# Optimization experiments

Hardware: AMD Instinct MI355X
Metric: run time of the kernel (lower is better)

The kernel has to match this reference:

```python
import jax, jax.numpy as jnp
import numpy as np

VOCAB = 50257
D = 256
N_UTT = 64
L = 512


def gru_scan(x, W_ih, W_hh, b_ih, b_hh):
    # torch nn.GRU (single layer, batch_first) semantics.
    # x: [B, T, d] -> outputs [B, T, d]
    B, T, d = x.shape
    gx = jnp.einsum('btd,gd->btg', x, W_ih) + b_ih  # [B, T, 3d] input gates precomputed
    gx = jnp.transpose(gx, (1, 0, 2))               # [T, B, 3d] for scan over time

    def step(h, gxt):
        gh = h @ W_hh.T + b_hh                      # [B, 3d]
        xr, xz, xn = jnp.split(gxt, 3, axis=-1)
        hr, hz, hn = jnp.split(gh, 3, axis=-1)
        r = jax.nn.sigmoid(xr + hr)
        z = jax.nn.sigmoid(xz + hz)
        n = jnp.tanh(xn + r * hn)
        h_new = (1.0 - z) * n + z * h
        return h_new, h_new

    h0 = jnp.zeros((B, d), x.dtype)
    _, hs = jax.lax.scan(step, h0, gx)              # hs: [T, B, d]
    return jnp.transpose(hs, (1, 0, 2))


def attn_pool(out, w, b):
    # out: [B, T, d]; Linear(d,1) -> softmax over T -> weighted sum
    logits = out @ w + b                            # [B, T]
    weights = jax.nn.softmax(logits, axis=-1)
    return jnp.einsum('bt,btd->bd', weights, out)   # [B, d]


def setup_inputs() -> dict:
    key = jax.random.key(0)
    ks = jax.random.split(key, 16)
    s = 1.0 / np.sqrt(D)
    u = lambda k, shape: jax.random.uniform(k, shape, jnp.float32, -s, s)
    return {
        'tokens': jax.random.randint(ks[0], (N_UTT, L), 0, VOCAB, dtype=jnp.int32),
        'embed': jax.random.normal(ks[1], (VOCAB, D), jnp.float32),
        'wg_Wih': u(ks[2], (3 * D, D)),
        'wg_Whh': u(ks[3], (3 * D, D)),
        'wg_bih': u(ks[4], (3 * D,)),
        'wg_bhh': u(ks[5], (3 * D,)),
        'ua_w': u(ks[6], (D,)),
        'ua_b': u(ks[7], ()),
        'sg_Wih': u(ks[8], (3 * D, D)),
        'sg_Whh': u(ks[9], (3 * D, D)),
        'sg_bih': u(ks[10], (3 * D,)),
        'sg_bhh': u(ks[11], (3 * D,)),
        'da_w': u(ks[12], (D,)),
        'da_b': u(ks[13], ()),
    }


def reference(tokens, embed, wg_Wih, wg_Whh, wg_bih, wg_bhh, ua_w, ua_b,
              sg_Wih, sg_Whh, sg_bih, sg_bhh, da_w, da_b):
    # Word level: embed each utterance, GRU, attention pooling (batched over utterances)
    emb = embed[tokens]                                   # [N, L, d]
    word_out = gru_scan(emb, wg_Wih, wg_Whh, wg_bih, wg_bhh)
    utt_vecs = attn_pool(word_out, ua_w, ua_b)            # [N, d]
    # Sentence level: pad_sequence of [1,d] vectors -> [N, 1, d] (batch=N, seq=1)
    sent_in = utt_vecs[:, None, :]                        # [N, 1, d]
    sent_out = gru_scan(sent_in, sg_Wih, sg_Whh, sg_bih, sg_bhh)
    dialog_vec = attn_pool(sent_out, da_w, da_b)          # [N, d] (softmax over seq len 1)
    return dialog_vec
```

## Files before the change

kernel.cpp:

```cpp
#include <hip/hip_runtime.h>

typedef _Float16 f16x8 __attribute__((ext_vector_type(8)));
typedef float f32x4 __attribute__((ext_vector_type(4)));

constexpr int D = 256;
constexpr int NUTT = 64;
constexpr int L = 512;
constexpr int G = 768;
constexpr int CHUNK = 128;
constexpr int NCH = L / CHUNK;
constexpr int NBLK = 6;
constexpr int NGEMM = NCH * NUTT * NBLK;

__device__ __forceinline__ void lds_barrier() {
  asm volatile("s_waitcnt lgkmcnt(0)\n\ts_barrier" ::: "memory");
}

__device__ __forceinline__ float fast_rcp(float x) {
  return __builtin_amdgcn_rcpf(x);
}
__device__ __forceinline__ float sigm(float x) {
  return fast_rcp(1.0f + __expf(-x));
}
__device__ __forceinline__ float tanh_f(float x) {
  float ax = fabsf(x);
  float e = __expf(-2.0f * ax);
  float r = (1.0f - e) * fast_rcp(1.0f + e);
  return copysignf(r, x);
}

__global__ __launch_bounds__(256) void pack_wih(
    const float* __restrict__ Wih, _Float16* __restrict__ hi,
    _Float16* __restrict__ lo, int* cnt) {
  if (blockIdx.x == 0) cnt[threadIdx.x << 4] = 0;
  const int e = blockIdx.x * 256 + threadIdx.x;
  const int g = e >> 8, k = e & 255;
  float v = Wih[e];
  _Float16 h = (_Float16)v;
  _Float16 l = (_Float16)(v - (float)h);
  const int it = g >> 4, l15 = g & 15;
  const int f = k >> 5, r = k & 31, lk = r >> 3, j = r & 7;
  const int dst = ((((it * 8 + f) * 4 + lk) * 16 + l15) * 8) + j;
  hi[dst] = h;
  lo[dst] = l;
}

__global__ __launch_bounds__(512, 2) void hran_mega(
    const int* __restrict__ tokens, const float* __restrict__ embed,
    const _Float16* __restrict__ whi, const _Float16* __restrict__ wlo,
    const float* __restrict__ bih,
    const float* __restrict__ Whh,
    const float* __restrict__ bhh,
    const float* __restrict__ uaw,
    const float* __restrict__ sWih, const float* __restrict__ sbih,
    const float* __restrict__ sbhh,
    float* __restrict__ gx,
    int* cnt,
    float* __restrict__ out) {
  __shared__ __align__(16) _Float16 hbuf[2][D];
  __shared__ float pre[3][D];
  __shared__ float lg[L];
  __shared__ float red[16];
  __shared__ float part[D];
  __shared__ float ut[D];

  const int bx = blockIdx.x;
  const int t = threadIdx.x;
  const int w = t >> 6;
  const int lane = t & 63;
  const int l15 = lane & 15;
  const int lk = lane >> 4;

  if (bx >= NUTT) {
    const int gbx = bx - NUTT;
    const int c = gbx / (NUTT * NBLK);
    const int rem = gbx % (NUTT * NBLK);
    const int u = rem / NBLK;
    const int nb = rem % NBLK;
    const int m0 = u * L + c * CHUNK;
    const int n0 = nb * 128;
    const int it0 = nb * 8;

    const int tok = tokens[m0 + 16 * w + l15];
    const float* arow = embed + (size_t)tok * D;
    const f16x8* Bh = (const f16x8*)whi;
    const f16x8* Bl = (const f16x8*)wlo;
    const int fragbase = lk * 16 + l15;

    f32x4 acc[8] = {};
#pragma unroll
    for (int f = 0; f < 8; ++f) {
      const float* ap = arow + 32 * f + 8 * lk;
      float4 v0 = *(const float4*)(ap);
      float4 v1 = *(const float4*)(ap + 4);
      float av[8] = {v0.x, v0.y, v0.z, v0.w, v1.x, v1.y, v1.z, v1.w};
      f16x8 ahi, alo;
#pragma unroll
      for (int j = 0; j < 8; ++j) {
        _Float16 h = (_Float16)av[j];
        ahi[j] = h;
        alo[j] = (_Float16)(av[j] - (float)h);
      }
#pragma unroll
      for (int i = 0; i < 8; ++i) {
        const int frag = ((it0 + i) * 8 + f) * 64 + fragbase;
        f16x8 bhi = Bh[frag];
        f16x8 blo = Bl[frag];
        acc[i] = __builtin_amdgcn_mfma_f32_16x16x32_f16(ahi, bhi, acc[i], 0, 0, 0);
        acc[i] = __builtin_amdgcn_mfma_f32_16x16x32_f16(alo, bhi, acc[i], 0, 0, 0);
        acc[i] = __builtin_amdgcn_mfma_f32_16x16x32_f16(ahi, blo, acc[i], 0, 0, 0);
      }
    }
#pragma unroll
    for (int i = 0; i < 8; ++i) {
      const int n = n0 + 16 * i + l15;
      const float bb = bih[n];
#pragma unroll
      for (int reg = 0; reg < 4; ++reg) {
        const int m = m0 + 16 * w + 4 * lk + reg;
        gx[(size_t)m * G + n] = acc[i][reg] + bb;
      }
    }
    __syncthreads();
    if (t == 0)
      __hip_atomic_fetch_add(&cnt[((u << 2) + c) << 4], 1,
                             __ATOMIC_RELEASE, __HIP_MEMORY_SCOPE_AGENT);
    return;
  }

  const int b = bx;

  f16x8 Bf[6][8];
#pragma unroll
  for (int i = 0; i < 6; ++i) {
    const float* row = Whh + (size_t)(96 * w + 16 * i + l15) * D + 8 * lk;
#pragma unroll
    for (int f = 0; f < 8; ++f) {
      float4 v0 = *(const float4*)(row + 32 * f);
      float4 v1 = *(const float4*)(row + 32 * f + 4);
      Bf[i][f] = f16x8{(_Float16)v0.x, (_Float16)v0.y,
                       (_Float16)v0.z, (_Float16)v0.w,
                       (_Float16)v1.x, (_Float16)v1.y,
                       (_Float16)v1.z, (_Float16)v1.w};
    }
  }

  float bR = 0.0f, bZ = 0.0f, bN = 0.0f;
  float gr = 0.0f, gz = 0.0f, gn = 0.0f;
  float hprev = 0.0f;
  float* gxb = gx + (size_t)b * L * G;
  if (t < 256) {
    bR = bhh[t]; bZ = bhh[D + t]; bN = bhh[2 * D + t];
    hbuf[0][t] = (_Float16)0.0f;
  }
  __syncthreads();

  for (int c = 0; c < NCH; ++c) {
    if (t == 0) {
      while (__hip_atomic_load(&cnt[((b << 2) + c) << 4],
                               __ATOMIC_ACQUIRE,
                               __HIP_MEMORY_SCOPE_AGENT) < NBLK)
        __builtin_amdgcn_s_sleep(8);
    }
    __syncthreads();
    __threadfence();
    if (t < 256) {
      const float* gc = gxb + (size_t)(CHUNK * c) * G;
      gr = gc[t]; gz = gc[D + t]; gn = gc[2 * D + t];
    }

    for (int tsl = 0; tsl < CHUNK; ++tsl) {
      const int ts = CHUNK * c + tsl;
      const int cur = ts & 1;
      const _Float16* hb = hbuf[cur];
      f16x8 A[8];
#pragma unroll
      for (int f = 0; f < 8; ++f)
        A[f] = *(const f16x8*)(hb + 32 * f + 8 * lk);

#pragma unroll
      for (int i = 0; i < 6; ++i) {
        f32x4 acc = {0.0f, 0.0f, 0.0f, 0.0f};
#pragma unroll
        for (int f = 0; f < 8; ++f)
          acc = __builtin_amdgcn_mfma_f32_16x16x32_f16(A[f], Bf[i][f], acc,
                                                       0, 0, 0);
        if (lk == 0) {
          const int n = 96 * w + 16 * i + l15;
          pre[n >> 8][n & 255] = acc[0];
        }
      }
      lds_barrier();

      if (t < 256) {
        float aR = pre[0][t], aZ = pre[1][t], aN = pre[2][t];
        float r = sigm(gr + aR + bR);
        float z = sigm(gz + aZ + bZ);
        float nn = tanh_f(gn + r * (aN + bN));
        float hn = fmaf(z, hprev - nn, nn);
        hprev = hn;
        hbuf[cur ^ 1][t] = (_Float16)hn;
        gxb[(size_t)ts * G + t] = hn;
        const int tn = ts + 1;
        if (tn & (CHUNK - 1)) {
          const float* gxn = gxb + (size_t)tn * G;
          gr = gxn[t]; gz = gxn[D + t]; gn = gxn[2 * D + t];
        }
      }
      lds_barrier();
    }
  }

  asm volatile("s_waitcnt vmcnt(0)" ::: "memory");
  __syncthreads();

  {
    const float ua0 = uaw[lane], ua1 = uaw[lane + 64];
    const float ua2 = uaw[lane + 128], ua3 = uaw[lane + 192];
    for (int r = 0; r < 64; ++r) {
      const int tt = 64 * w + r;
      const float* row = gxb + (size_t)tt * G;
      float p = row[lane] * ua0 + row[lane + 64] * ua1 +
                row[lane + 128] * ua2 + row[lane + 192] * ua3;
#pragma unroll
      for (int off = 32; off; off >>= 1) p += __shfl_down(p, off);
      if (lane == 0) lg[tt] = p;
    }
  }
  __syncthreads();

  {
    float v = lg[t];
    float m = v;
#pragma unroll
    for (int off = 32; off; off >>= 1) m = fmaxf(m, __shfl_xor(m, off));
    if (lane == 0) red[w] = m;
    __syncthreads();
    m = red[0];
#pragma unroll
    for (int i = 1; i < 8; ++i) m = fmaxf(m, red[i]);
    float e = __expf(v - m);
    float s = e;
#pragma unroll
    for (int off = 32; off; off >>= 1) s += __shfl_xor(s, off);
    if (lane == 0) red[8 + w] = s;
    __syncthreads();
    s = red[8];
#pragma unroll
    for (int i = 9; i < 16; ++i) s += red[i];
    lg[t] = e * (1.0f / s);
  }
  __syncthreads();

  {
    const int d = t & 255, half = t >> 8;
    float acc = 0.0f;
    const float* bb = gxb + (size_t)half * 256 * G;
    const float* lgh = lg + half * 256;
#pragma unroll 4
    for (int k = 0; k < 256; ++k)
      acc = fmaf(lgh[k], bb[(size_t)k * G + d], acc);
    if (half == 1) part[d] = acc;
    __syncthreads();
    if (half == 0) ut[d] = acc + part[d];
    __syncthreads();
  }

  if (t < 256) {
    const int d = t;
    const float* wr = sWih + (size_t)d * D;
    const float* wz = sWih + (size_t)(D + d) * D;
    const float* wn = sWih + (size_t)(2 * D + d) * D;
    float ar = 0.0f, az = 0.0f, an = 0.0f;
    for (int k = 0; k < D; k += 4) {
      float4 vr = *(const float4*)(wr + k);
      float4 vz = *(const float4*)(wz + k);
      float4 vn = *(const float4*)(wn + k);
      float u0 = ut[k], u1 = ut[k + 1], u2 = ut[k + 2], u3 = ut[k + 3];
      ar += vr.x * u0 + vr.y * u1 + vr.z * u2 + vr.w * u3;
      az += vz.x * u0 + vz.y * u1 + vz.z * u2 + vz.w * u3;
      an += vn.x * u0 + vn.y * u1 + vn.z * u2 + vn.w * u3;
    }
    float r = sigm(ar + sbih[d] + sbhh[d]);
    float z = sigm(az + sbih[D + d] + sbhh[D + d]);
    float n = tanh_f(an + sbih[2 * D + d] + r * sbhh[2 * D + d]);
    out[(size_t)b * D + d] = (1.0f - z) * n;
  }
}

extern "C" void kernel_launch(void* const* d_in, const int* in_sizes, int n_in,
                              void* d_out, int out_size, void* d_ws, size_t ws_size,
                              hipStream_t stream) {
  const int* tokens    = (const int*)d_in[0];
  const float* embed   = (const float*)d_in[1];
  const float* wg_Wih  = (const float*)d_in[2];
  const float* wg_Whh  = (const float*)d_in[3];
  const float* wg_bih  = (const float*)d_in[4];
  const float* wg_bhh  = (const float*)d_in[5];
  const float* ua_w    = (const float*)d_in[6];
  const float* sg_Wih  = (const float*)d_in[8];
  const float* sg_bih  = (const float*)d_in[10];
  const float* sg_bhh  = (const float*)d_in[11];
  float* out = (float*)d_out;

  char* ws = (char*)d_ws;
  const size_t GXB = (size_t)NUTT * L * G * 4;
  float* gx = (float*)ws;
  _Float16* whi = (_Float16*)(ws + GXB);
  _Float16* wlo = whi + (size_t)G * D;
  int* cnt = (int*)(ws + GXB + (size_t)2 * G * D * 2);

  pack_wih<<<G, 256, 0, stream>>>(wg_Wih, whi, wlo, cnt);
  hran_mega<<<NUTT + NGEMM, 512, 0, stream>>>(
      tokens, embed, whi, wlo, wg_bih, wg_Whh, wg_bhh, ua_w,
      sg_Wih, sg_bih, sg_bhh, gx, cnt, out);
}
```

Baseline: 784.0 us.

## Fuse attention pooling into GRU loop with online softmax on idle wave

The word-level attention pooling now runs inside the recurrent loop. An otherwise idle wavefront reads each new hidden state from an fp32 LDS copy and keeps a running max, sum and weighted accumulator, an online softmax. This removes the per-step global stores of hidden states and the three later passes over them: logits, softmax and weighted sum. The weight pack kernel is also reindexed so writes are contiguous and reads are gathered. The cost is more LDS, plus exp work on the idle wave that competes for issue slots on the critical serial loop.

Result: slower. 843.7 us (+7.6%).

```diff
diff --git a/kernel.cpp b/kernel.cpp
--- a/kernel.cpp
+++ b/kernel.cpp
@@ -33,16 +33,18 @@
     const float* __restrict__ Wih, _Float16* __restrict__ hi,
     _Float16* __restrict__ lo, int* cnt) {
   if (blockIdx.x == 0) cnt[threadIdx.x << 4] = 0;
-  const int e = blockIdx.x * 256 + threadIdx.x;
-  const int g = e >> 8, k = e & 255;
-  float v = Wih[e];
+  const int d = blockIdx.x * 256 + threadIdx.x;
+  const int j = d & 7;
+  const int l15 = (d >> 3) & 15;
+  const int lk = (d >> 7) & 3;
+  const int f = (d >> 9) & 7;
+  const int it = d >> 12;
+  const int g = 16 * it + l15;
+  const int k = 32 * f + 8 * lk + j;
+  float v = Wih[g * 256 + k];
   _Float16 h = (_Float16)v;
-  _Float16 l = (_Float16)(v - (float)h);
-  const int it = g >> 4, l15 = g & 15;
-  const int f = k >> 5, r = k & 31, lk = r >> 3, j = r & 7;
-  const int dst = ((((it * 8 + f) * 4 + lk) * 16 + l15) * 8) + j;
-  hi[dst] = h;
-  lo[dst] = l;
+  hi[d] = h;
+  lo[d] = (_Float16)(v - (float)h);
 }
 
 __global__ __launch_bounds__(512, 2) void hran_mega(
@@ -58,11 +60,9 @@
     int* cnt,
     float* __restrict__ out) {
   __shared__ __align__(16) _Float16 hbuf[2][D];
+  __shared__ __align__(16) float hbuf32[2][D];
   __shared__ float pre[3][D];
-  __shared__ float lg[L];
-  __shared__ float red[16];
-  __shared__ float part[D];
-  __shared__ float ut[D];
+  __shared__ __align__(16) float ut[D];
 
   const int bx = blockIdx.x;
   const int t = threadIdx.x;
@@ -153,6 +153,11 @@
     bR = bhh[t]; bZ = bhh[D + t]; bN = bhh[2 * D + t];
     hbuf[0][t] = (_Float16)0.0f;
   }
+
+  float am = -1e30f, aS = 0.0f;
+  float4 aN = {0.0f, 0.0f, 0.0f, 0.0f};
+  float4 uav = {0.0f, 0.0f, 0.0f, 0.0f};
+  if (w == 4) uav = *(const float4*)(uaw + 4 * lane);
   __syncthreads();
 
   for (int c = 0; c < NCH; ++c) {
@@ -193,78 +198,56 @@
       lds_barrier();
 
       if (t < 256) {
-        float aR = pre[0][t], aZ = pre[1][t], aN = pre[2][t];
+        float aR = pre[0][t], aZ = pre[1][t], aNp = pre[2][t];
         float r = sigm(gr + aR + bR);
         float z = sigm(gz + aZ + bZ);
-        float nn = tanh_f(gn + r * (aN + bN));
+        float nn = tanh_f(gn + r * (aNp + bN));
         float hn = fmaf(z, hprev - nn, nn);
         hprev = hn;
         hbuf[cur ^ 1][t] = (_Float16)hn;
-        gxb[(size_t)ts * G + t] = hn;
+        hbuf32[cur ^ 1][t] = hn;
         const int tn = ts + 1;
         if (tn & (CHUNK - 1)) {
           const float* gxn = gxb + (size_t)tn * G;
           gr = gxn[t]; gz = gxn[D + t]; gn = gxn[2 * D + t];
         }
+      } else if (w == 4 && ts > 0) {
+        float4 hv = *(const float4*)(&hbuf32[cur][4 * lane]);
+        float lp = hv.x * uav.x + hv.y * uav.y + hv.z * uav.z + hv.w * uav.w;
+#pragma unroll
+        for (int off = 32; off; off >>= 1) lp += __shfl_xor(lp, off);
+        float mn = fmaxf(am, lp);
+        float cs = __expf(am - mn);
+        float wg = __expf(lp - mn);
+        aS = aS * cs + wg;
+        aN.x = aN.x * cs + wg * hv.x;
+        aN.y = aN.y * cs + wg * hv.y;
+        aN.z = aN.z * cs + wg * hv.z;
+        aN.w = aN.w * cs + wg * hv.w;
+        am = mn;
       }
       lds_barrier();
     }
   }
 
-  asm volatile("s_waitcnt vmcnt(0)" ::: "memory");
+  if (w == 4) {
+    float4 hv = *(const float4*)(&hbuf32[0][4 * lane]);
+    float lp = hv.x * uav.x + hv.y * uav.y + hv.z * uav.z + hv.w * uav.w;
+#pragma unroll
+    for (int off = 32; off; off >>= 1) lp += __shfl_xor(lp, off);
+    float mn = fmaxf(am, lp);
+    float cs = __expf(am - mn);
+    float wg = __expf(lp - mn);
+    aS = aS * cs + wg;
+    aN.x = aN.x * cs + wg * hv.x;
+    aN.y = aN.y * cs + wg * hv.y;
+    aN.z = aN.z * cs + wg * hv.z;
+    aN.w = aN.w * cs + wg * hv.w;
+    float inv = 1.0f / aS;
+    float4 uo = {aN.x * inv, aN.y * inv, aN.z * inv, aN.w * inv};
+    *(float4*)(&ut[4 * lane]) = uo;
+  }
   __syncthreads();
-
-  {
-    const float ua0 = uaw[lane], ua1 = uaw[lane + 64];
-    const float ua2 = uaw[lane + 128], ua3 = uaw[lane + 192];
-    for (int r = 0; r < 64; ++r) {
-      const int tt = 64 * w + r;
-      const float* row = gxb + (size_t)tt * G;
-      float p = row[lane] * ua0 + row[lane + 64] * ua1 +
-                row[lane + 128] * ua2 + row[lane + 192] * ua3;
-#pragma unroll
-      for (int off = 32; off; off >>= 1) p += __shfl_down(p, off);
-      if (lane == 0) lg[tt] = p;
-    }
-  }
-  __syncthreads();
-
-  {
-    float v = lg[t];
-    float m = v;
-#pragma unroll
-    for (int off = 32; off; off >>= 1) m = fmaxf(m, __shfl_xor(m, off));
-    if (lane == 0) red[w] = m;
-    __syncthreads();
-    m = red[0];
-#pragma unroll
-    for (int i = 1; i < 8; ++i) m = fmaxf(m, red[i]);
-    float e = __expf(v - m);
-    float s = e;
-#pragma unroll
-    for (int off = 32; off; off >>= 1) s += __shfl_xor(s, off);
-    if (lane == 0) red[8 + w] = s;
-    __syncthreads();
-    s = red[8];
-#pragma unroll
-    for (int i = 9; i < 16; ++i) s += red[i];
-    lg[t] = e * (1.0f / s);
-  }
-  __syncthreads();
-
-  {
-    const int d = t & 255, half = t >> 8;
-    float acc = 0.0f;
-    const float* bb = gxb + (size_t)half * 256 * G;
-    const float* lgh = lg + half * 256;
-#pragma unroll 4
-    for (int k = 0; k < 256; ++k)
-      acc = fmaf(lgh[k], bb[(size_t)k * G + d], acc);
-    if (half == 1) part[d] = acc;
-    __syncthreads();
-    if (half == 0) ut[d] = acc + part[d];
-    __syncthreads();
-  }
 
   if (t < 256) {
     const int d = t;
```

## Overlap attention logits with GRU recurrence and store word outputs as fp16

Applied to the files above, without the earlier changes.

During the recurrent loop, the four idle waves now compute per-timestep attention logit partials from an fp32 copy of the hidden state kept in LDS. This replaces the separate post-loop pass that re-read every hidden state from global memory. Word-level outputs are written to a separate compact fp16 buffer, which the weighted pooling reads instead of strided fp32 rows, and pack_wih now makes coalesced writes by iterating over the destination index. The cost is extra LDS and fp16 rounding in the pooled sum.

Measured after the change: 836.8 us. 6.7% more time.

```diff
diff --git a/kernel.cpp b/kernel.cpp
--- a/kernel.cpp
+++ b/kernel.cpp
@@ -33,16 +33,18 @@
     const float* __restrict__ Wih, _Float16* __restrict__ hi,
     _Float16* __restrict__ lo, int* cnt) {
   if (blockIdx.x == 0) cnt[threadIdx.x << 4] = 0;
-  const int e = blockIdx.x * 256 + threadIdx.x;
-  const int g = e >> 8, k = e & 255;
-  float v = Wih[e];
+  const int d = blockIdx.x * 256 + threadIdx.x;
+  const int j = d & 7;
+  const int l15 = (d >> 3) & 15;
+  const int lk = (d >> 7) & 3;
+  const int f = (d >> 9) & 7;
+  const int it = d >> 12;
+  const int g = 16 * it + l15;
+  const int k = 32 * f + 8 * lk + j;
+  float v = Wih[g * 256 + k];
   _Float16 h = (_Float16)v;
-  _Float16 l = (_Float16)(v - (float)h);
-  const int it = g >> 4, l15 = g & 15;
-  const int f = k >> 5, r = k & 31, lk = r >> 3, j = r & 7;
-  const int dst = ((((it * 8 + f) * 4 + lk) * 16 + l15) * 8) + j;
-  hi[dst] = h;
-  lo[dst] = l;
+  hi[d] = h;
+  lo[d] = (_Float16)(v - (float)h);
 }
 
 __global__ __launch_bounds__(512, 2) void hran_mega(
@@ -55,14 +57,17 @@
     const float* __restrict__ sWih, const float* __restrict__ sbih,
     const float* __restrict__ sbhh,
     float* __restrict__ gx,
+    _Float16* __restrict__ wo16,
     int* cnt,
     float* __restrict__ out) {
   __shared__ __align__(16) _Float16 hbuf[2][D];
+  __shared__ __align__(16) float hbuf32[2][D];
   __shared__ float pre[3][D];
+  __shared__ float plg[L][4];
   __shared__ float lg[L];
   __shared__ float red[16];
   __shared__ float part[D];
-  __shared__ float ut[D];
+  __shared__ __align__(16) float ut[D];
 
   const int bx = blockIdx.x;
   const int t = threadIdx.x;
@@ -149,10 +154,14 @@
   float gr = 0.0f, gz = 0.0f, gn = 0.0f;
   float hprev = 0.0f;
   float* gxb = gx + (size_t)b * L * G;
+  _Float16* wob = wo16 + (size_t)b * L * D;
   if (t < 256) {
     bR = bhh[t]; bZ = bhh[D + t]; bN = bhh[2 * D + t];
     hbuf[0][t] = (_Float16)0.0f;
   }
+  const int q = w - 4;
+  float uaq = 0.0f;
+  if (w >= 4) uaq = uaw[64 * q + lane];
   __syncthreads();
 
   for (int c = 0; c < NCH; ++c) {
@@ -193,40 +202,39 @@
       lds_barrier();
 
       if (t < 256) {
-        float aR = pre[0][t], aZ = pre[1][t], aN = pre[2][t];
+        float aR = pre[0][t], aZ = pre[1][t], aNp = pre[2][t];
         float r = sigm(gr + aR + bR);
         float z = sigm(gz + aZ + bZ);
-        float nn = tanh_f(gn + r * (aN + bN));
+        float nn = tanh_f(gn + r * (aNp + bN));
         float hn = fmaf(z, hprev - nn, nn);
         hprev = hn;
-        hbuf[cur ^ 1][t] = (_Float16)hn;
-        gxb[(size_t)ts * G + t] = hn;
+        _Float16 hf = (_Float16)hn;
+        hbuf[cur ^ 1][t] = hf;
+        hbuf32[cur ^ 1][t] = hn;
+        wob[(size_t)ts * D + t] = hf;
         const int tn = ts + 1;
         if (tn & (CHUNK - 1)) {
           const float* gxn = gxb + (size_t)tn * G;
           gr = gxn[t]; gz = gxn[D + t]; gn = gxn[2 * D + t];
         }
+      } else if (ts > 0) {
+        float p = hbuf32[cur][64 * q + lane] * uaq;
+#pragma unroll
+        for (int off = 32; off; off >>= 1) p += __shfl_xor(p, off);
+        if (lane == 0) plg[ts - 1][q] = p;
       }
       lds_barrier();
     }
   }
 
-  asm volatile("s_waitcnt vmcnt(0)" ::: "memory");
+  if (w >= 4) {
+    float p = hbuf32[0][64 * q + lane] * uaq;
+#pragma unroll
+    for (int off = 32; off; off >>= 1) p += __shfl_xor(p, off);
+    if (lane == 0) plg[511][q] = p;
+  }
   __syncthreads();
-
-  {
-    const float ua0 = uaw[lane], ua1 = uaw[lane + 64];
-    const float ua2 = uaw[lane + 128], ua3 = uaw[lane + 192];
-    for (int r = 0; r < 64; ++r) {
-      const int tt = 64 * w + r;
-      const float* row = gxb + (size_t)tt * G;
-      float p = row[lane] * ua0 + row[lane + 64] * ua1 +
-                row[lane + 128] * ua2 + row[lane + 192] * ua3;
-#pragma unroll
-      for (int off = 32; off; off >>= 1) p += __shfl_down(p, off);
-      if (lane == 0) lg[tt] = p;
-    }
-  }
+  lg[t] = plg[t][0] + plg[t][1] + plg[t][2] + plg[t][3];
   __syncthreads();
 
   {
@@ -253,13 +261,14 @@
   __syncthreads();
 
   {
+    asm volatile("s_waitcnt vmcnt(0)" ::: "memory");
     const int d = t & 255, half = t >> 8;
     float acc = 0.0f;
-    const float* bb = gxb + (size_t)half * 256 * G;
+    const _Float16* bbp = wob + (size_t)half * 256 * D;
     const float* lgh = lg + half * 256;
 #pragma unroll 4
     for (int k = 0; k < 256; ++k)
-      acc = fmaf(lgh[k], bb[(size_t)k * G + d], acc);
+      acc = fmaf(lgh[k], (float)bbp[(size_t)k * D + d], acc);
     if (half == 1) part[d] = acc;
     __syncthreads();
     if (half == 0) ut[d] = acc + part[d];
@@ -309,9 +318,10 @@
   _Float16* whi = (_Float16*)(ws + GXB);
   _Float16* wlo = whi + (size_t)G * D;
   int* cnt = (int*)(ws + GXB + (size_t)2 * G * D * 2);
+  _Float16* wo16 = (_Float16*)(ws + GXB + (size_t)2 * G * D * 2 + 16384);
 
   pack_wih<<<G, 256, 0, stream>>>(wg_Wih, whi, wlo, cnt);
   hran_mega<<<NUTT + NGEMM, 512, 0, stream>>>(
       tokens, embed, whi, wlo, wg_bih, wg_Whh, wg_bhh, ua_w,
-      sg_Wih, sg_bih, sg_bhh, gx, cnt, out);
-}
+      sg_Wih, sg_bih, sg_bhh, gx, wo16, cnt, out);
+}
```
